# Performance work log

Hardware: AMD Instinct MI355X
Metric: run time of the kernel (lower is better)

## Reference

```python
import jax, jax.numpy as jnp
import numpy as np
from jax import lax

B, T, D, H = 2048, 512, 88, 16


def setup_inputs() -> dict:
    key = jax.random.key(0)
    k1, k2, k3, k4 = jax.random.split(key, 4)
    # binary piano-roll observations [num_sequences, max_length, data_dim]
    sequences = (jax.random.uniform(k1, (B, T, D)) < 0.5).astype(jnp.float32)
    # simplex transition matrix [H, H]
    probs_x = jax.nn.softmax(jax.random.normal(k2, (H, H)), axis=-1)
    # unit-interval emission probs [H, D]
    probs_y = jax.nn.sigmoid(jax.random.normal(k3, (H, D)))
    lengths = jax.random.randint(k4, (B,), 1, T + 1).astype(jnp.int32)
    mb = jnp.arange(B, dtype=jnp.int64)
    mask = jnp.ones((B,), dtype=bool)
    scale = jnp.float32(1.0)
    return {"sequences": sequences, "probs_x": probs_x, "probs_y": probs_y,
            "scale": scale, "lengths": lengths, "mb": mb, "mask": mask}


def reference(sequences, probs_x, probs_y, scale, lengths, mb, mask):
    # Minibatch selection (mb indexes sequences/lengths, as in the pyro model)
    seq = sequences[mb]            # [B, T, D]
    lens = lengths[mb]             # [B]
    log_A = jnp.log(probs_x)       # [H, H] transition log-probs
    log_py = jnp.log(probs_y)      # [H, D]
    log_1mpy = jnp.log1p(-probs_y)
    # Bernoulli emission log-likelihood summed over tones plate: [B, T, H]
    emit = (jnp.einsum('btd,hd->bth', seq, log_py)
            + jnp.einsum('btd,hd->bth', 1.0 - seq, log_1mpy))
    NEG = jnp.float32(-1e30)
    # x starts at state 0 before the first transition -> delta at state 0
    alpha0 = jnp.full((seq.shape[0], log_A.shape[0]), NEG).at[:, 0].set(0.0)

    def step(alpha, inp):
        emit_t, t = inp            # emit_t: [B, H]
        nxt = jax.nn.logsumexp(alpha[:, :, None] + log_A[None], axis=1) + emit_t
        valid = (t < lens)[:, None]  # handlers.mask(t < lengths)
        return jnp.where(valid, nxt, alpha), None

    emit_tbh = jnp.swapaxes(emit, 0, 1)          # [T, B, H]
    alphaT, _ = lax.scan(step, alpha0, (emit_tbh, jnp.arange(emit_tbh.shape[0])))
    ll = jax.nn.logsumexp(alphaT, axis=-1)       # marginal log-lik per sequence
    # sequences-plate mask + handlers.scale
    return scale * jnp.where(mask, ll, 0.0)
```

## Files before the change

kernel.cpp:

```cpp
#include <hip/hip_runtime.h>

#define B_N 2048
#define T_N 512
#define D_N 88
#define H_N 16
#define NEGF (-1e30f)
#define LN2F 0.69314718055994530942f

template<int CTRL>
__device__ __forceinline__ float dppf(float x) {
    return __int_as_float(__builtin_amdgcn_update_dpp(
        0, __float_as_int(x), CTRL, 0xF, 0xF, false));
}

__device__ __forceinline__ float grp16_max(float v) {
    v = fmaxf(v, dppf<0x128>(v));
    v = fmaxf(v, dppf<0x124>(v));
    v = fmaxf(v, dppf<0x122>(v));
    v = fmaxf(v, dppf<0x121>(v));
    return v;
}
__device__ __forceinline__ float grp16_sum(float v) {
    v += dppf<0x128>(v);
    v += dppf<0x124>(v);
    v += dppf<0x122>(v);
    v += dppf<0x121>(v);
    return v;
}

__device__ __forceinline__ void calib(const float* __restrict__ px, int h,
                                      float (&aro)[16]) {
    float idxf = (float)h;
    aro[0]  = px[h * 16 + h];
    aro[1]  = px[((int)dppf<0x121>(idxf)) * 16 + h];
    aro[2]  = px[((int)dppf<0x122>(idxf)) * 16 + h];
    aro[3]  = px[((int)dppf<0x123>(idxf)) * 16 + h];
    aro[4]  = px[((int)dppf<0x124>(idxf)) * 16 + h];
    aro[5]  = px[((int)dppf<0x125>(idxf)) * 16 + h];
    aro[6]  = px[((int)dppf<0x126>(idxf)) * 16 + h];
    aro[7]  = px[((int)dppf<0x127>(idxf)) * 16 + h];
    aro[8]  = px[((int)dppf<0x128>(idxf)) * 16 + h];
    aro[9]  = px[((int)dppf<0x129>(idxf)) * 16 + h];
    aro[10] = px[((int)dppf<0x12A>(idxf)) * 16 + h];
    aro[11] = px[((int)dppf<0x12B>(idxf)) * 16 + h];
    aro[12] = px[((int)dppf<0x12C>(idxf)) * 16 + h];
    aro[13] = px[((int)dppf<0x12D>(idxf)) * 16 + h];
    aro[14] = px[((int)dppf<0x12E>(idxf)) * 16 + h];
    aro[15] = px[((int)dppf<0x12F>(idxf)) * 16 + h];
}

__device__ __forceinline__ float matvec16(float p, const float (&aro)[16]) {
    float a0 = p * aro[0];
    float a1 = dppf<0x121>(p) * aro[1];
    float a2 = dppf<0x122>(p) * aro[2];
    float a3 = dppf<0x123>(p) * aro[3];
    a0 += dppf<0x124>(p) * aro[4];
    a1 += dppf<0x125>(p) * aro[5];
    a2 += dppf<0x126>(p) * aro[6];
    a3 += dppf<0x127>(p) * aro[7];
    a0 += dppf<0x128>(p) * aro[8];
    a1 += dppf<0x129>(p) * aro[9];
    a2 += dppf<0x12A>(p) * aro[10];
    a3 += dppf<0x12B>(p) * aro[11];
    a0 += dppf<0x12C>(p) * aro[12];
    a1 += dppf<0x12D>(p) * aro[13];
    a2 += dppf<0x12E>(p) * aro[14];
    a3 += dppf<0x12F>(p) * aro[15];
    return (a0 + a1) + (a2 + a3);
}

__device__ __forceinline__ void hmm_step(float& aRel, float& M, float emit2,
                                         bool valid, const float (&aro)[16]) {
    float p = exp2f(aRel);
    float s = matvec16(p, aro);
    float g = __log2f(s) + emit2;
    float mg = grp16_max(g);
    if (valid) {
        aRel = g - mg;
        M    = M + mg;
    }
}

__global__ void hmm_prep(const float* __restrict__ probs_y,
                         float* __restrict__ wtab) {
    int tid = threadIdx.x;
    for (int i = tid; i < H_N * D_N; i += 256) {
        float py = probs_y[i];
        wtab[i] = log2f(py) - log2f(1.0f - py);
    }
    if (tid < H_N) {
        float s = 0.0f;
        for (int d = 0; d < D_N; ++d)
            s += log2f(1.0f - probs_y[tid * D_N + d]);
        wtab[H_N * D_N + tid] = s;
    }
}

__global__ __launch_bounds__(256) void hmm_emit(
    const float* __restrict__ seq, const int* __restrict__ lengths,
    const float* __restrict__ wtab, float* __restrict__ emitBuf) {
    int bid = blockIdx.x;
    int b = bid >> 3;
    int t0 = (bid & 7) * 64;
    int len = lengths[b];
    if (t0 >= len) return;

    __shared__ float sW[H_N * D_N + H_N];
    __shared__ float sS[64 * 92];
    int tid = threadIdx.x;

    for (int i = tid; i < H_N * D_N + H_N; i += 256) sW[i] = wtab[i];

    const float4* gs = (const float4*)(seq + ((size_t)b * T_N + t0) * D_N);
    for (int f = tid; f < 64 * 22; f += 256) {
        float4 v = gs[f];
        int row = f / 22, j = f - row * 22;
        *(float4*)(&sS[row * 92 + j * 4]) = v;
    }
    __syncthreads();

    int row = tid & 63, hq = tid >> 6;
    int t = t0 + row;
    if (t >= len) return;

    const float* srow = &sS[row * 92];
    const float* w0 = &sW[(hq * 4 + 0) * D_N];
    const float* w1 = &sW[(hq * 4 + 1) * D_N];
    const float* w2 = &sW[(hq * 4 + 2) * D_N];
    const float* w3 = &sW[(hq * 4 + 3) * D_N];
    const float* bb = &sW[H_N * D_N];
    float a0 = bb[hq * 4 + 0], a1 = bb[hq * 4 + 1];
    float a2 = bb[hq * 4 + 2], a3 = bb[hq * 4 + 3];
#pragma unroll
    for (int j = 0; j < 22; ++j) {
        float4 sv = *(const float4*)(srow + 4 * j);
        float4 q0 = *(const float4*)(w0 + 4 * j);
        float4 q1 = *(const float4*)(w1 + 4 * j);
        float4 q2 = *(const float4*)(w2 + 4 * j);
        float4 q3 = *(const float4*)(w3 + 4 * j);
        a0 += sv.x * q0.x + sv.y * q0.y + sv.z * q0.z + sv.w * q0.w;
        a1 += sv.x * q1.x + sv.y * q1.y + sv.z * q1.z + sv.w * q1.w;
        a2 += sv.x * q2.x + sv.y * q2.y + sv.z * q2.z + sv.w * q2.w;
        a3 += sv.x * q3.x + sv.y * q3.y + sv.z * q3.z + sv.w * q3.w;
    }
    size_t ob = ((size_t)b * H_N + hq * 4) * T_N + t;
    emitBuf[ob]           = a0;
    emitBuf[ob + T_N]     = a1;
    emitBuf[ob + 2 * T_N] = a2;
    emitBuf[ob + 3 * T_N] = a3;
}

__global__ __launch_bounds__(64) void hmm_scan(
    const float* __restrict__ probs_x, const float* __restrict__ emitBuf,
    const int* __restrict__ lengths, const float* __restrict__ scale,
    float* __restrict__ out) {
    int lane = threadIdx.x;
    int sl = lane >> 4, h = lane & 15;
    int b0 = blockIdx.x * 4;
    int b = b0 + sl;
    int len = lengths[b];

    float aro[16];
    calib(probs_x, h, aro);

    int wmax = max(max(lengths[b0], lengths[b0 + 1]),
                   max(lengths[b0 + 2], lengths[b0 + 3]));

    const float4* eb = (const float4*)(emitBuf + ((size_t)(b * H_N + h)) * T_N);
    float aRel = (h == 0) ? 0.0f : NEGF;
    float M = 0.0f;

    int nch = (wmax + 3) >> 2;
    float4 cur = eb[0];
    for (int c = 0; c < nch; ++c) {
        float4 nxt;
        if (c + 1 < nch) nxt = eb[c + 1];
        int t0c = c * 4;
        hmm_step(aRel, M, cur.x, t0c + 0 < len, aro);
        hmm_step(aRel, M, cur.y, t0c + 1 < len, aro);
        hmm_step(aRel, M, cur.z, t0c + 2 < len, aro);
        hmm_step(aRel, M, cur.w, t0c + 3 < len, aro);
        cur = nxt;
    }
    float pf = exp2f(aRel);
    float s = grp16_sum(pf);
    if (h == 0)
        out[b] = scale[0] * (LN2F * (M + __log2f(s)));
}

__global__ __launch_bounds__(64) void hmm_fused_naive(
    const float* __restrict__ seq, const float* __restrict__ px,
    const float* __restrict__ py, const float* __restrict__ sc,
    const int* __restrict__ lengths, float* __restrict__ out) {
    int lane = threadIdx.x;
    int sl = lane >> 4, h = lane & 15;
    int b0 = blockIdx.x * 4;
    int b = b0 + sl;
    int len = lengths[b];

    float aro[16];
    calib(px, h, aro);

    float wreg[88];
    float b2 = 0.0f;
#pragma unroll
    for (int d = 0; d < D_N; ++d) {
        float p = py[h * D_N + d];
        float l1 = log2f(1.0f - p);
        wreg[d] = log2f(p) - l1;
        b2 += l1;
    }
    int wmax = max(max(lengths[b0], lengths[b0 + 1]),
                   max(lengths[b0 + 2], lengths[b0 + 3]));

    float aRel = (h == 0) ? 0.0f : NEGF;
    float M = 0.0f;
    for (int t = 0; t < wmax; ++t) {
        const float4* sp = (const float4*)(seq + ((size_t)b * T_N + t) * D_N);
        float e = b2;
#pragma unroll
        for (int j = 0; j < 22; ++j) {
            float4 v = sp[j];
            e += v.x * wreg[4 * j] + v.y * wreg[4 * j + 1] +
                 v.z * wreg[4 * j + 2] + v.w * wreg[4 * j + 3];
        }
        hmm_step(aRel, M, e, t < len, aro);
    }
    float pf = exp2f(aRel);
    float s = grp16_sum(pf);
    if (h == 0)
        out[b] = sc[0] * (LN2F * (M + __log2f(s)));
}

extern "C" void kernel_launch(void* const* d_in, const int* in_sizes, int n_in,
                              void* d_out, int out_size, void* d_ws,
                              size_t ws_size, hipStream_t stream) {
    const float* seq = (const float*)d_in[0];
    const float* px  = (const float*)d_in[1];
    const float* py  = (const float*)d_in[2];
    const float* sc  = (const float*)d_in[3];
    const int*   len = (const int*)d_in[4];
    float* out = (float*)d_out;

    size_t emit_elems = (size_t)B_N * H_N * T_N;
    size_t need = (emit_elems + (H_N * D_N + H_N)) * sizeof(float);
    if (ws_size >= need) {
        float* emitBuf = (float*)d_ws;
        float* wtab = emitBuf + emit_elems;
        hmm_prep<<<1, 256, 0, stream>>>(py, wtab);
        hmm_emit<<<B_N * 8, 256, 0, stream>>>(seq, len, wtab, emitBuf);
        hmm_scan<<<B_N / 4, 64, 0, stream>>>(px, emitBuf, len, sc, out);
    } else {
        hmm_fused_naive<<<B_N / 4, 64, 0, stream>>>(seq, px, py, sc, len, out);
    }
}
```

Before: 606.0 us.

## Compute emissions with bf16 MFMA and hoist per-step max normalization out of scan

```diff
diff --git a/kernel.cpp b/kernel.cpp
--- a/kernel.cpp
+++ b/kernel.cpp
@@ -6,6 +6,9 @@
 #define H_N 16
 #define NEGF (-1e30f)
 #define LN2F 0.69314718055994530942f
+
+typedef __attribute__((ext_vector_type(8))) short short8;
+typedef __attribute__((ext_vector_type(4))) float floatx4;
 
 template<int CTRL>
 __device__ __forceinline__ float dppf(float x) {
@@ -69,91 +72,121 @@
     return (a0 + a1) + (a2 + a3);
 }
 
+__device__ __forceinline__ void scan_step(float& aRel, float& M, float ec,
+                                          float cval, bool valid,
+                                          const float (&aro)[16]) {
+    float p = exp2f(aRel);
+    float s = matvec16(p, aro);
+    float g = __log2f(s) + ec;
+    if (valid) { aRel = g; M += cval; }
+}
+
 __device__ __forceinline__ void hmm_step(float& aRel, float& M, float emit2,
                                          bool valid, const float (&aro)[16]) {
     float p = exp2f(aRel);
     float s = matvec16(p, aro);
     float g = __log2f(s) + emit2;
     float mg = grp16_max(g);
-    if (valid) {
-        aRel = g - mg;
-        M    = M + mg;
-    }
+    if (valid) { aRel = g - mg; M = M + mg; }
 }
 
 __global__ void hmm_prep(const float* __restrict__ probs_y,
-                         float* __restrict__ wtab) {
+                         ushort* __restrict__ bpack, float* __restrict__ base) {
     int tid = threadIdx.x;
-    for (int i = tid; i < H_N * D_N; i += 256) {
-        float py = probs_y[i];
-        wtab[i] = log2f(py) - log2f(1.0f - py);
+    for (int i = tid; i < 3 * 64 * 8; i += 256) {
+        int k = i >> 9;
+        int l = (i >> 3) & 63;
+        int j = i & 7;
+        int kk = k * 32 + ((l >> 4) * 8) + j;
+        int h = l & 15;
+        ushort v = 0;
+        if (kk < D_N) {
+            float p = probs_y[h * D_N + kk];
+            float lw = log2f(p) - log2f(1.0f - p);
+            unsigned u = __float_as_uint(lw);
+            u += 0x7FFFu + ((u >> 16) & 1u);
+            v = (ushort)(u >> 16);
+        }
+        bpack[i] = v;
     }
     if (tid < H_N) {
         float s = 0.0f;
         for (int d = 0; d < D_N; ++d)
             s += log2f(1.0f - probs_y[tid * D_N + d]);
-        wtab[H_N * D_N + tid] = s;
+        base[tid] = s;
     }
 }
 
 __global__ __launch_bounds__(256) void hmm_emit(
     const float* __restrict__ seq, const int* __restrict__ lengths,
-    const float* __restrict__ wtab, float* __restrict__ emitBuf) {
+    const ushort* __restrict__ bpack, const float* __restrict__ base,
+    float* __restrict__ ecBuf, float* __restrict__ cBuf) {
     int bid = blockIdx.x;
     int b = bid >> 3;
     int t0 = (bid & 7) * 64;
-    int len = lengths[b];
-    if (t0 >= len) return;
-
-    __shared__ float sW[H_N * D_N + H_N];
-    __shared__ float sS[64 * 92];
+    if (t0 >= lengths[b]) return;
+
+    __shared__ ushort sA[64 * 104];
     int tid = threadIdx.x;
-
-    for (int i = tid; i < H_N * D_N + H_N; i += 256) sW[i] = wtab[i];
-
-    const float4* gs = (const float4*)(seq + ((size_t)b * T_N + t0) * D_N);
-    for (int f = tid; f < 64 * 22; f += 256) {
-        float4 v = gs[f];
-        int row = f / 22, j = f - row * 22;
-        *(float4*)(&sS[row * 92 + j * 4]) = v;
+    const float* gseq = seq + ((size_t)b * T_N + t0) * D_N;
+
+    for (int f = tid; f < 768; f += 256) {
+        if (f < 704) {
+            int r = f / 11;
+            int c = f - r * 11;
+            const float* gp = gseq + f * 8;
+            float4 v0 = *(const float4*)(gp);
+            float4 v1 = *(const float4*)(gp + 4);
+            uint4 w;
+            w.x = (__float_as_uint(v0.x) >> 16) | (__float_as_uint(v0.y) & 0xFFFF0000u);
+            w.y = (__float_as_uint(v0.z) >> 16) | (__float_as_uint(v0.w) & 0xFFFF0000u);
+            w.z = (__float_as_uint(v1.x) >> 16) | (__float_as_uint(v1.y) & 0xFFFF0000u);
+            w.w = (__float_as_uint(v1.z) >> 16) | (__float_as_uint(v1.w) & 0xFFFF0000u);
+            *(uint4*)(&sA[r * 104 + c * 8]) = w;
+        } else {
+            int r = f - 704;
+            uint4 z; z.x = 0; z.y = 0; z.z = 0; z.w = 0;
+            *(uint4*)(&sA[r * 104 + 88]) = z;
+        }
     }
     __syncthreads();
 
-    int row = tid & 63, hq = tid >> 6;
-    int t = t0 + row;
-    if (t >= len) return;
-
-    const float* srow = &sS[row * 92];
-    const float* w0 = &sW[(hq * 4 + 0) * D_N];
-    const float* w1 = &sW[(hq * 4 + 1) * D_N];
-    const float* w2 = &sW[(hq * 4 + 2) * D_N];
-    const float* w3 = &sW[(hq * 4 + 3) * D_N];
-    const float* bb = &sW[H_N * D_N];
-    float a0 = bb[hq * 4 + 0], a1 = bb[hq * 4 + 1];
-    float a2 = bb[hq * 4 + 2], a3 = bb[hq * 4 + 3];
-#pragma unroll
-    for (int j = 0; j < 22; ++j) {
-        float4 sv = *(const float4*)(srow + 4 * j);
-        float4 q0 = *(const float4*)(w0 + 4 * j);
-        float4 q1 = *(const float4*)(w1 + 4 * j);
-        float4 q2 = *(const float4*)(w2 + 4 * j);
-        float4 q3 = *(const float4*)(w3 + 4 * j);
-        a0 += sv.x * q0.x + sv.y * q0.y + sv.z * q0.z + sv.w * q0.w;
-        a1 += sv.x * q1.x + sv.y * q1.y + sv.z * q1.z + sv.w * q1.w;
-        a2 += sv.x * q2.x + sv.y * q2.y + sv.z * q2.z + sv.w * q2.w;
-        a3 += sv.x * q3.x + sv.y * q3.y + sv.z * q3.z + sv.w * q3.w;
-    }
-    size_t ob = ((size_t)b * H_N + hq * 4) * T_N + t;
-    emitBuf[ob]           = a0;
-    emitBuf[ob + T_N]     = a1;
-    emitBuf[ob + 2 * T_N] = a2;
-    emitBuf[ob + 3 * T_N] = a3;
+    int l = tid & 63, w = tid >> 6;
+    int q = l >> 4, h = l & 15;
+
+    const short8* bp = (const short8*)bpack;
+    short8 bf0 = bp[l];
+    short8 bf1 = bp[64 + l];
+    short8 bf2 = bp[128 + l];
+
+    int arow = w * 16 + h;
+    short8 af0 = *(const short8*)&sA[arow * 104 + 0  + q * 8];
+    short8 af1 = *(const short8*)&sA[arow * 104 + 32 + q * 8];
+    short8 af2 = *(const short8*)&sA[arow * 104 + 64 + q * 8];
+
+    floatx4 acc = {0.f, 0.f, 0.f, 0.f};
+    acc = __builtin_amdgcn_mfma_f32_16x16x32_bf16(af0, bf0, acc, 0, 0, 0);
+    acc = __builtin_amdgcn_mfma_f32_16x16x32_bf16(af1, bf1, acc, 0, 0, 0);
+    acc = __builtin_amdgcn_mfma_f32_16x16x32_bf16(af2, bf2, acc, 0, 0, 0);
+
+    float bh = base[h];
+    float e0 = acc[0] + bh, e1 = acc[1] + bh, e2 = acc[2] + bh, e3 = acc[3] + bh;
+    float c0 = grp16_max(e0), c1 = grp16_max(e1);
+    float c2 = grp16_max(e2), c3 = grp16_max(e3);
+
+    int tloc = t0 + w * 16 + q * 4;
+    float4 ecv; ecv.x = e0 - c0; ecv.y = e1 - c1; ecv.z = e2 - c2; ecv.w = e3 - c3;
+    *(float4*)&ecBuf[((size_t)(b * H_N + h)) * T_N + tloc] = ecv;
+    if (h == 0) {
+        float4 cv; cv.x = c0; cv.y = c1; cv.z = c2; cv.w = c3;
+        *(float4*)&cBuf[(size_t)b * T_N + tloc] = cv;
+    }
 }
 
 __global__ __launch_bounds__(64) void hmm_scan(
-    const float* __restrict__ probs_x, const float* __restrict__ emitBuf,
-    const int* __restrict__ lengths, const float* __restrict__ scale,
-    float* __restrict__ out) {
+    const float* __restrict__ probs_x, const float* __restrict__ ecBuf,
+    const float* __restrict__ cBuf, const int* __restrict__ lengths,
+    const float* __restrict__ scale, float* __restrict__ out) {
     int lane = threadIdx.x;
     int sl = lane >> 4, h = lane & 15;
     int b0 = blockIdx.x * 4;
@@ -166,21 +199,25 @@
     int wmax = max(max(lengths[b0], lengths[b0 + 1]),
                    max(lengths[b0 + 2], lengths[b0 + 3]));
 
-    const float4* eb = (const float4*)(emitBuf + ((size_t)(b * H_N + h)) * T_N);
+    const float4* eb = (const float4*)(ecBuf + ((size_t)(b * H_N + h)) * T_N);
+    const float4* cb = (const float4*)(cBuf + (size_t)b * T_N);
     float aRel = (h == 0) ? 0.0f : NEGF;
     float M = 0.0f;
 
     int nch = (wmax + 3) >> 2;
-    float4 cur = eb[0];
+    float4 e0 = eb[0], e1 = eb[1];
+    float4 g0 = cb[0], g1 = cb[1];
     for (int c = 0; c < nch; ++c) {
-        float4 nxt;
-        if (c + 1 < nch) nxt = eb[c + 1];
+        float4 e2 = eb[c + 2];
+        float4 g2 = cb[c + 2];
         int t0c = c * 4;
-        hmm_step(aRel, M, cur.x, t0c + 0 < len, aro);
-        hmm_step(aRel, M, cur.y, t0c + 1 < len, aro);
-        hmm_step(aRel, M, cur.z, t0c + 2 < len, aro);
-        hmm_step(aRel, M, cur.w, t0c + 3 < len, aro);
-        cur = nxt;
+        scan_step(aRel, M, e0.x, g0.x, t0c + 0 < len, aro);
+        scan_step(aRel, M, e0.y, g0.y, t0c + 1 < len, aro);
+        scan_step(aRel, M, e0.z, g0.z, t0c + 2 < len, aro);
+        scan_step(aRel, M, e0.w, g0.w, t0c + 3 < len, aro);
+        float mg = grp16_max(aRel);
+        aRel -= mg; M += mg;
+        e0 = e1; e1 = e2; g0 = g1; g1 = g2;
     }
     float pf = exp2f(aRel);
     float s = grp16_sum(pf);
@@ -242,14 +279,17 @@
     const int*   len = (const int*)d_in[4];
     float* out = (float*)d_out;
 
-    size_t emit_elems = (size_t)B_N * H_N * T_N;
-    size_t need = (emit_elems + (H_N * D_N + H_N)) * sizeof(float);
+    size_t ec_elems = (size_t)B_N * H_N * T_N;
+    size_t c_elems  = (size_t)B_N * T_N;
+    size_t need = (ec_elems + c_elems + 16) * sizeof(float) + 1536 * sizeof(ushort);
     if (ws_size >= need) {
-        float* emitBuf = (float*)d_ws;
-        float* wtab = emitBuf + emit_elems;
-        hmm_prep<<<1, 256, 0, stream>>>(py, wtab);
-        hmm_emit<<<B_N * 8, 256, 0, stream>>>(seq, len, wtab, emitBuf);
-        hmm_scan<<<B_N / 4, 64, 0, stream>>>(px, emitBuf, len, sc, out);
+        float*  ecBuf = (float*)d_ws;
+        float*  cBuf  = ecBuf + ec_elems;
+        float*  base  = cBuf + c_elems;
+        ushort* bpack = (ushort*)(base + 16);
+        hmm_prep<<<1, 256, 0, stream>>>(py, bpack, base);
+        hmm_emit<<<B_N * 8, 256, 0, stream>>>(seq, len, bpack, base, ecBuf, cBuf);
+        hmm_scan<<<B_N / 4, 64, 0, stream>>>(px, ecBuf, cBuf, len, sc, out);
     } else {
         hmm_fused_naive<<<B_N / 4, 64, 0, stream>>>(seq, px, py, sc, len, out);
     }
```

Result: faster. 545.4 us (-10.0%).
